# Performance work log

Measured on AMD Instinct MI355X. Metric: run time of the kernel, lower is better.

## Reference

```python
import jax, jax.numpy as jnp
import numpy as np

# B images, N objects/image, R relations/image; D=obj/rel feature dim, H=GGNN hidden,
# NO=num object classes, NR=num relation classes, T=GGNN time steps.
B, N, R, D, H, NO, NR, T = 8, 64, 2048, 4096, 512, 151, 51, 3


def setup_inputs() -> dict:
    key = jax.random.key(0)
    ks = jax.random.split(key, 24)
    nrm = lambda k, shp: jax.random.normal(k, shp, dtype=jnp.float32) * 0.02
    im_inds = jnp.repeat(jnp.arange(B, dtype=jnp.int32), N)          # sorted per-object image ids
    img_r = jnp.repeat(jnp.arange(B, dtype=jnp.int32), R)            # per-relation image ids
    pair = jax.random.randint(ks[0], (B * R, 2), 0, N, dtype=jnp.int32) + (img_r * N)[:, None]
    rel_inds = jnp.concatenate([img_r[:, None], pair], axis=1)        # [B*R, 3]
    return dict(
        im_inds=im_inds, rel_inds=rel_inds,
        obj_fmaps=jax.random.normal(ks[1], (B * N, D), jnp.float32),
        obj_logits=jax.random.normal(ks[2], (B * N, NO), jnp.float32),
        vr=jax.random.normal(ks[3], (B * R, D), jnp.float32),
        W_obj=nrm(ks[4], (D, H)), b_obj=jnp.zeros((H,), jnp.float32),
        W_rel=nrm(ks[5], (D, H)), b_rel=jnp.zeros((H,), jnp.float32),
        W_prob=nrm(ks[6], (NO, H)), b_prob=jnp.zeros((H,), jnp.float32),
        W_so=nrm(ks[7], (H, H)), W_oo=nrm(ks[8], (H, H)),
        W_rs=nrm(ks[9], (H, H)), W_ro=nrm(ks[10], (H, H)),
        Wz=nrm(ks[11], (H, H)), Uz=nrm(ks[12], (H, H)), bz=jnp.zeros((H,), jnp.float32),
        Wr=nrm(ks[13], (H, H)), Ur=nrm(ks[14], (H, H)), br=jnp.zeros((H,), jnp.float32),
        Wh=nrm(ks[15], (H, H)), Uh=nrm(ks[16], (H, H)), bh=jnp.zeros((H,), jnp.float32),
        W_out_rel=nrm(ks[17], (2 * H, H)), b_out_rel=jnp.zeros((H,), jnp.float32),
        W_cls_rel=nrm(ks[18], (H, NR)), b_cls_rel=jnp.zeros((NR,), jnp.float32),
        W_out_obj=nrm(ks[19], (2 * H, H)), b_out_obj=jnp.zeros((H,), jnp.float32),
        W_cls_obj=nrm(ks[20], (H, NO)), b_cls_obj=jnp.zeros((NO,), jnp.float32),
    )


def reference(im_inds, rel_inds, obj_fmaps, obj_logits, vr,
              W_obj, b_obj, W_rel, b_rel, W_prob, b_prob,
              W_so, W_oo, W_rs, W_ro,
              Wz, Uz, bz, Wr, Ur, br, Wh, Uh, bh,
              W_out_rel, b_out_rel, W_cls_rel, b_cls_rel,
              W_out_obj, b_out_obj, W_cls_obj, b_cls_obj):
    # obj_probs = softmax(obj_logits); project features + class distribution into GGNN hidden
    obj_probs = jax.nn.softmax(obj_logits, axis=-1)
    xo = (obj_fmaps @ W_obj + b_obj + obj_probs @ W_prob + b_prob).reshape(B, N, H)
    xr = (vr @ W_rel + b_rel).reshape(B, R, H)
    # per-image local indices: rel_inds[rel_s:rel_e, 1:] - obj_s
    off = (jnp.arange(B, dtype=rel_inds.dtype) * N)[:, None]
    subj = rel_inds[:, 1].reshape(B, R) - off
    objn = rel_inds[:, 2].reshape(B, R) - off

    def gru(h, m):
        z = jax.nn.sigmoid(m @ Wz + h @ Uz + bz)
        r = jax.nn.sigmoid(m @ Wr + h @ Ur + br)
        hh = jnp.tanh(m @ Wh + (r * h) @ Uh + bh)
        return (1.0 - z) * h + z * hh

    def per_image(xo_i, xr_i, s, o):
        ho, hr = xo_i, xr_i
        for _ in range(T):  # fixed recurrence depth (time_step_num)
            mr = ho[s] @ W_so + ho[o] @ W_oo                               # gather obj -> rel
            mo = (jax.ops.segment_sum(hr @ W_rs, s, num_segments=N)
                  + jax.ops.segment_sum(hr @ W_ro, o, num_segments=N))     # scatter rel -> obj
            ho, hr = gru(ho, mo), gru(hr, mr)
        rel_logits = jnp.tanh(jnp.concatenate([hr, xr_i], -1) @ W_out_rel + b_out_rel) @ W_cls_rel + b_cls_rel
        obj_ref = jnp.tanh(jnp.concatenate([ho, xo_i], -1) @ W_out_obj + b_out_obj) @ W_cls_obj + b_cls_obj
        return rel_logits, obj_ref

    rel_logits, obj_ref = jax.vmap(per_image)(xo, xr, subj, objn)
    rel_logits = rel_logits.reshape(B * R, NR)
    obj_ref = obj_ref.reshape(B * N, NO)
    scpred_softmax = jax.nn.softmax(rel_logits, axis=-1)
    scent_softmax = jax.nn.softmax(obj_ref, axis=-1)
    # sgcls, inference, no obj_labels: obj_preds = argmax over classes 1..NO-1, + 1
    obj_preds = jnp.argmax(obj_ref[:, 1:], axis=-1) + 1
    return (obj_ref, obj_preds, rel_logits, scpred_softmax, scent_softmax)
```

## Files before the change

### kernel.cpp

```cpp
#include <hip/hip_runtime.h>
#include <math.h>

#define Bn   8
#define Nn   64
#define Rn   2048
#define Dn   4096
#define Hn   512
#define NOc  151
#define NRc  51
#define Tt   3
#define BNt  (Bn*Nn)
#define BRt  (Bn*Rn)

typedef __attribute__((ext_vector_type(8))) short short8;
typedef __attribute__((ext_vector_type(4))) float f32x4;

__device__ __forceinline__ float sigmf(float x){ return 1.0f/(1.0f+expf(-x)); }

__device__ __forceinline__ ushort f2bf_rne(float x){
  unsigned u = __float_as_uint(x);
  unsigned r = u + 0x7FFFu + ((u>>16)&1u);
  return (ushort)(r>>16);
}

template<int BM,int BN>
__global__ __launch_bounds__(256)
void gemm_b3(const float* __restrict__ A, const ushort* __restrict__ Bhg,
             const ushort* __restrict__ Blg, float* __restrict__ C,
             int M,int N,int K,int lda,int ldb,int ldc,
             const float* __restrict__ bias,int beta,int act)
{
  constexpr int MT = BM/32, NT = BN/32;
  __shared__ ushort Ah[BM*40], Al[BM*40], Bh[BN*40], Bl[BN*40];
  const int tid  = threadIdx.x;
  const int lane = tid & 63;
  const int wid  = tid >> 6;
  const int quad = lane >> 4, l15 = lane & 15;
  const int wm = (wid>>1)*(BM/2), wn = (wid&1)*(BN/2);
  const int bm = blockIdx.y*BM, bn = blockIdx.x*BN;

  constexpr int TPR  = 256/BM;
  constexpr int FPT  = 32/TPR;
  const int ar = tid / TPR;
  const int ak = (tid % TPR) * FPT;
  constexpr int TPRB = 256/BN;
  constexpr int SPT  = 32/TPRB;
  const int br = tid / TPRB;
  const int bk = (tid % TPRB) * SPT;
  const int grA = bm + ar;
  const int grB = bn + br;

  f32x4 acc[MT][NT];
#pragma unroll
  for (int i=0;i<MT;i++)
#pragma unroll
    for (int j=0;j<NT;j++) acc[i][j] = (f32x4){0.f,0.f,0.f,0.f};

  for (int k0=0; k0<K; k0+=32) {
    {
      float av[FPT];
      if (grA < M && k0 + ak + FPT <= K) {
        const float* p = A + (size_t)grA*lda + k0 + ak;
#pragma unroll
        for (int i=0;i<FPT/4;i++) ((float4*)av)[i] = ((const float4*)p)[i];
      } else {
#pragma unroll
        for (int i=0;i<FPT;i++){
          int gk = k0+ak+i;
          av[i] = (grA<M && gk<K) ? A[(size_t)grA*lda+gk] : 0.f;
        }
      }
      ushort hs[FPT], ls[FPT];
#pragma unroll
      for (int i=0;i<FPT;i++){
        ushort h = f2bf_rne(av[i]);
        float hf = __uint_as_float(((unsigned)h)<<16);
        hs[i]=h; ls[i]=f2bf_rne(av[i]-hf);
      }
#pragma unroll
      for (int i=0;i<FPT;i+=8){
        short8 vh, vl;
#pragma unroll
        for (int q=0;q<8;q++){ vh[q]=(short)hs[i+q]; vl[q]=(short)ls[i+q]; }
        *(short8*)&Ah[ar*40+ak+i] = vh;
        *(short8*)&Al[ar*40+ak+i] = vl;
      }
    }
    {
#pragma unroll
      for (int i=0;i<SPT;i+=8){
        short8 vh, vl;
        if (grB < N){
          vh = *(const short8*)(Bhg + (size_t)grB*ldb + k0 + bk + i);
          vl = *(const short8*)(Blg + (size_t)grB*ldb + k0 + bk + i);
        } else {
#pragma unroll
          for (int q=0;q<8;q++){ vh[q]=0; vl[q]=0; }
        }
        *(short8*)&Bh[br*40+bk+i] = vh;
        *(short8*)&Bl[br*40+bk+i] = vl;
      }
    }
    __syncthreads();
    {
      short8 afh[MT], afl[MT], bfh[NT], bfl[NT];
#pragma unroll
      for (int i=0;i<MT;i++){
        int o = (wm + i*16 + l15)*40 + quad*8;
        afh[i] = *(const short8*)&Ah[o];
        afl[i] = *(const short8*)&Al[o];
      }
#pragma unroll
      for (int j=0;j<NT;j++){
        int o = (wn + j*16 + l15)*40 + quad*8;
        bfh[j] = *(const short8*)&Bh[o];
        bfl[j] = *(const short8*)&Bl[o];
      }
#pragma unroll
      for (int i=0;i<MT;i++)
#pragma unroll
        for (int j=0;j<NT;j++)
          acc[i][j] = __builtin_amdgcn_mfma_f32_16x16x32_bf16(afh[i], bfh[j], acc[i][j], 0,0,0);
#pragma unroll
      for (int i=0;i<MT;i++)
#pragma unroll
        for (int j=0;j<NT;j++)
          acc[i][j] = __builtin_amdgcn_mfma_f32_16x16x32_bf16(afh[i], bfl[j], acc[i][j], 0,0,0);
#pragma unroll
      for (int i=0;i<MT;i++)
#pragma unroll
        for (int j=0;j<NT;j++)
          acc[i][j] = __builtin_amdgcn_mfma_f32_16x16x32_bf16(afl[i], bfh[j], acc[i][j], 0,0,0);
    }
    __syncthreads();
  }
#pragma unroll
  for (int i=0;i<MT;i++){
    int gm0 = bm + wm + i*16 + quad*4;
#pragma unroll
    for (int j=0;j<NT;j++){
      int gn = bn + wn + j*16 + l15;
      if (gn >= N) continue;
#pragma unroll
      for (int r=0;r<4;r++){
        int gm = gm0 + r;
        if (gm >= M) continue;
        float v = acc[i][j][r];
        if (beta) v += C[(size_t)gm*ldc+gn];
        if (bias) v += bias[gn];
        if (act==1) v = sigmf(v);
        else if (act==2) v = tanhf(v);
        C[(size_t)gm*ldc+gn] = v;
      }
    }
  }
}

__global__ __launch_bounds__(256)
void tsplit(const float* __restrict__ src,int K,int N,
            ushort* __restrict__ dh, ushort* __restrict__ dl,
            int dld,int rowoff,int koff)
{
  __shared__ float t[32][33];
  const int tx = threadIdx.x, ty = threadIdx.y;
  const int kb = blockIdx.x*32, nb = blockIdx.y*32;
#pragma unroll
  for (int r=0;r<4;r++){
    int k = kb + ty + r*8, n = nb + tx;
    t[ty+r*8][tx] = (k<K && n<N) ? src[(size_t)k*N + n] : 0.f;
  }
  __syncthreads();
#pragma unroll
  for (int r=0;r<4;r++){
    int n = nb + ty + r*8, k = kb + tx;
    if (n < N){
      float v = t[tx][ty+r*8];
      ushort h = f2bf_rne(v);
      float hf = __uint_as_float(((unsigned)h)<<16);
      ushort l = f2bf_rne(v - hf);
      size_t o = (size_t)(rowoff+n)*dld + koff + k;
      dh[o]=h; dl[o]=l;
    }
  }
}

__global__ __launch_bounds__(64)
void softmax_kernel(const float* __restrict__ in, float* __restrict__ out,
                    int cols, int ldi, int ldo, int padto)
{
  int row = blockIdx.x, lane = threadIdx.x;
  const float* rp = in + (size_t)row*ldi;
  float m = -INFINITY;
  for (int c = lane; c < cols; c += 64) m = fmaxf(m, rp[c]);
  for (int off = 32; off; off >>= 1) m = fmaxf(m, __shfl_xor(m, off));
  float s = 0.f;
  for (int c = lane; c < cols; c += 64) s += expf(rp[c]-m);
  for (int off = 32; off; off >>= 1) s += __shfl_xor(s, off);
  float inv = 1.f/s;
  float* op = out + (size_t)row*ldo;
  for (int c = lane; c < padto; c += 64)
    op[c] = (c < cols) ? expf(rp[c]-m)*inv : 0.f;
}

__global__ __launch_bounds__(64)
void argmax_kernel(const float* __restrict__ ref, float* __restrict__ preds)
{
  int row = blockIdx.x, lane = threadIdx.x;
  const float* rp = ref + (size_t)row*NOc;
  float bv = -INFINITY; int bi = NOc;
  for (int c = 1+lane; c < NOc; c += 64) { float v = rp[c]; if (v > bv) { bv=v; bi=c; } }
  for (int off=32; off; off>>=1) {
    float ov = __shfl_xor(bv, off); int oi = __shfl_xor(bi, off);
    if (ov > bv || (ov == bv && oi < bi)) { bv = ov; bi = oi; }
  }
  if (lane==0) preds[row] = (float)bi;
}

__global__ __launch_bounds__(256)
void copy512(float* __restrict__ dst, const float* __restrict__ src, int M)
{
  int i = blockIdx.x*256+threadIdx.x;
  if (i >= M*128) return;
  int row=i>>7, hq=(i&127)<<2;
  *(float4*)&dst[(size_t)row*1024+hq] = *(const float4*)&src[(size_t)row*1024+hq];
}

__global__ __launch_bounds__(64)
void segsum2(const float* __restrict__ HX, const int* __restrict__ rel_inds,
             float* __restrict__ SumSO)
{
  __shared__ float accS[64][64];
  __shared__ float accO[64][64];
  const int t = threadIdx.x;
  const int hb = blockIdx.x*64;
  const int img = blockIdx.z;
  const int relbase = img*Rn + blockIdx.y*(Rn/4);
  for (int ob=0; ob<64; ob++){ accS[ob][t]=0.f; accO[ob][t]=0.f; }
  for (int i=0;i<Rn/4;i++){
    int r = relbase+i;
    int s = rel_inds[r*3+1] - img*64;
    int o = rel_inds[r*3+2] - img*64;
    float v = HX[(size_t)r*1024 + hb + t];
    accS[s][t]+=v; accO[o][t]+=v;
  }
  for (int ob=0;ob<64;ob++){
    size_t rowb = (size_t)(img*64+ob)*1024 + hb + t;
    atomicAdd(&SumSO[rowb],     accS[ob][t]);
    atomicAdd(&SumSO[rowb+512], accO[ob][t]);
  }
}

__global__ __launch_bounds__(256)
void gru_rel_A2(const int* __restrict__ rel, const float* __restrict__ Gso,
                const float* __restrict__ hU, const float* __restrict__ HX,
                const float* __restrict__ bz, const float* __restrict__ br,
                float* __restrict__ Z, float* __restrict__ RH)
{
  int i = blockIdx.x*256 + threadIdx.x;
  if (i >= BRt*128) return;
  int r = i>>7, hq = (i&127)<<2;
  int s = rel[r*3+1], o = rel[r*3+2];
  float4 gzs = *(const float4*)&Gso[(size_t)s*3072 + hq];
  float4 gzo = *(const float4*)&Gso[(size_t)o*3072 + 1536 + hq];
  float4 grs = *(const float4*)&Gso[(size_t)s*3072 + 512 + hq];
  float4 gro = *(const float4*)&Gso[(size_t)o*3072 + 2048 + hq];
  float4 uz  = *(const float4*)&hU[(size_t)r*1024 + hq];
  float4 ur  = *(const float4*)&hU[(size_t)r*1024 + 512 + hq];
  float4 bzv = *(const float4*)&bz[hq];
  float4 brv = *(const float4*)&br[hq];
  float4 hv  = *(const float4*)&HX[(size_t)r*1024 + hq];
  float4 z, rh;
  z.x = sigmf(gzs.x+gzo.x+uz.x+bzv.x);
  z.y = sigmf(gzs.y+gzo.y+uz.y+bzv.y);
  z.z = sigmf(gzs.z+gzo.z+uz.z+bzv.z);
  z.w = sigmf(gzs.w+gzo.w+uz.w+bzv.w);
  rh.x = sigmf(grs.x+gro.x+ur.x+brv.x)*hv.x;
  rh.y = sigmf(grs.y+gro.y+ur.y+brv.y)*hv.y;
  rh.z = sigmf(grs.z+gro.z+ur.z+brv.z)*hv.z;
  rh.w = sigmf(grs.w+gro.w+ur.w+brv.w)*hv.w;
  *(float4*)&Z[(size_t)r*512+hq]  = z;
  *(float4*)&RH[(size_t)r*512+hq] = rh;
}

__global__ __launch_bounds__(256)
void gru_rel_B2(const int* __restrict__ rel, const float* __restrict__ Gso,
                const float* __restrict__ rhU, const float* __restrict__ Z,
                const float* __restrict__ bh, float* __restrict__ HX)
{
  int i = blockIdx.x*256 + threadIdx.x;
  if (i >= BRt*128) return;
  int r = i>>7, hq = (i&127)<<2;
  int s = rel[r*3+1], o = rel[r*3+2];
  float4 ghs = *(const float4*)&Gso[(size_t)s*3072 + 1024 + hq];
  float4 gho = *(const float4*)&Gso[(size_t)o*3072 + 2560 + hq];
  float4 ru  = *(const float4*)&rhU[(size_t)r*512 + hq];
  float4 bhv = *(const float4*)&bh[hq];
  float4 z   = *(const float4*)&Z[(size_t)r*512 + hq];
  float4 hv  = *(const float4*)&HX[(size_t)r*1024 + hq];
  float4 o4;
  o4.x = (1.f-z.x)*hv.x + z.x*tanhf(ghs.x+gho.x+ru.x+bhv.x);
  o4.y = (1.f-z.y)*hv.y + z.y*tanhf(ghs.y+gho.y+ru.y+bhv.y);
  o4.z = (1.f-z.z)*hv.z + z.z*tanhf(ghs.z+gho.z+ru.z+bhv.z);
  o4.w = (1.f-z.w)*hv.w + z.w*tanhf(ghs.w+gho.w+ru.w+bhv.w);
  *(float4*)&HX[(size_t)r*1024+hq] = o4;
}

__global__ __launch_bounds__(256)
void obj_gate(const float* __restrict__ G1, const float* __restrict__ G2,
              const float* __restrict__ HOX, const float* __restrict__ bz,
              const float* __restrict__ br, float* __restrict__ Zo,
              float* __restrict__ RHo)
{
  int i = blockIdx.x*256 + threadIdx.x;
  if (i >= BNt*128) return;
  int row = i>>7, hq = (i&127)<<2;
  float4 g1z = *(const float4*)&G1[(size_t)row*1536 + hq];
  float4 g2z = *(const float4*)&G2[(size_t)row*1024 + hq];
  float4 g1r = *(const float4*)&G1[(size_t)row*1536 + 512 + hq];
  float4 g2r = *(const float4*)&G2[(size_t)row*1024 + 512 + hq];
  float4 bzv = *(const float4*)&bz[hq];
  float4 brv = *(const float4*)&br[hq];
  float4 hv  = *(const float4*)&HOX[(size_t)row*1024 + hq];
  float4 z, rh;
  z.x = sigmf(g1z.x+g2z.x+bzv.x); z.y = sigmf(g1z.y+g2z.y+bzv.y);
  z.z = sigmf(g1z.z+g2z.z+bzv.z); z.w = sigmf(g1z.w+g2z.w+bzv.w);
  rh.x = sigmf(g1r.x+g2r.x+brv.x)*hv.x;
  rh.y = sigmf(g1r.y+g2r.y+brv.y)*hv.y;
  rh.z = sigmf(g1r.z+g2r.z+brv.z)*hv.z;
  rh.w = sigmf(g1r.w+g2r.w+brv.w)*hv.w;
  *(float4*)&Zo[(size_t)row*512+hq]  = z;
  *(float4*)&RHo[(size_t)row*512+hq] = rh;
}

__global__ __launch_bounds__(256)
void obj_upd(const float* __restrict__ G1, const float* __restrict__ rhUo,
             const float* __restrict__ Zo, const float* __restrict__ bh,
             float* __restrict__ HOX)
{
  int i = blockIdx.x*256 + threadIdx.x;
  if (i >= BNt*128) return;
  int row = i>>7, hq = (i&127)<<2;
  float4 g1h = *(const float4*)&G1[(size_t)row*1536 + 1024 + hq];
  float4 ru  = *(const float4*)&rhUo[(size_t)row*512 + hq];
  float4 z   = *(const float4*)&Zo[(size_t)row*512 + hq];
  float4 bhv = *(const float4*)&bh[hq];
  float4 hv  = *(const float4*)&HOX[(size_t)row*1024 + hq];
  float4 o4;
  o4.x = (1.f-z.x)*hv.x + z.x*tanhf(g1h.x+ru.x+bhv.x);
  o4.y = (1.f-z.y)*hv.y + z.y*tanhf(g1h.y+ru.y+bhv.y);
  o4.z = (1.f-z.z)*hv.z + z.z*tanhf(g1h.z+ru.z+bhv.z);
  o4.w = (1.f-z.w)*hv.w + z.w*tanhf(g1h.w+ru.w+bhv.w);
  *(float4*)&HOX[(size_t)row*1024+hq] = o4;
}

static void G128(hipStream_t s,const float*A,const ushort*bh,const ushort*bl,float*C,
  int M,int N,int K,int lda,int ldb,int ldc,const float*bias,int beta,int act){
  dim3 g((N+127)/128,(M+127)/128);
  gemm_b3<128,128><<<g,256,0,s>>>(A,bh,bl,C,M,N,K,lda,ldb,ldc,bias,beta,act);
}
static void G64(hipStream_t s,const float*A,const ushort*bh,const ushort*bl,float*C,
  int M,int N,int K,int lda,int ldb,int ldc,const float*bias,int beta,int act){
  dim3 g((N+63)/64,(M+63)/64);
  gemm_b3<64,64><<<g,256,0,s>>>(A,bh,bl,C,M,N,K,lda,ldb,ldc,bias,beta,act);
}
static void G128x64(hipStream_t s,const float*A,const ushort*bh,const ushort*bl,float*C,
  int M,int N,int K,int lda,int ldb,int ldc,const float*bias,int beta,int act){
  dim3 g((N+63)/64,(M+127)/128);
  gemm_b3<128,64><<<g,256,0,s>>>(A,bh,bl,C,M,N,K,lda,ldb,ldc,bias,beta,act);
}
static void TS(hipStream_t s,const float*src,int K,int N,ushort*dh,ushort*dl,
               int dld,int rowoff,int koff,int Kpad){
  dim3 g(Kpad/32,(N+31)/32);
  tsplit<<<g,dim3(32,8),0,s>>>(src,K,N,dh,dl,dld,rowoff,koff);
}

extern "C" void kernel_launch(void* const* d_in, const int* in_sizes, int n_in,
                              void* d_out, int out_size, void* d_ws, size_t ws_size,
                              hipStream_t stream) {
  (void)in_sizes; (void)n_in; (void)out_size; (void)ws_size;
  const int*   rel_inds   = (const int*)  d_in[1];
  const float* obj_fmaps  = (const float*)d_in[2];
  const float* obj_logits = (const float*)d_in[3];
  const float* vr         = (const float*)d_in[4];
  const float* W_obj      = (const float*)d_in[5];
  const float* b_obj      = (const float*)d_in[6];
  const float* W_rel      = (const float*)d_in[7];
  const float* b_rel      = (const float*)d_in[8];
  const float* W_prob     = (const float*)d_in[9];
  const float* b_prob     = (const float*)d_in[10];
  const float* W_so       = (const float*)d_in[11];
  const float* W_oo       = (const float*)d_in[12];
  const float* W_rs       = (const float*)d_in[13];
  const float* W_ro       = (const float*)d_in[14];
  const float* Wz         = (const float*)d_in[15];
  const float* Uz         = (const float*)d_in[16];
  const float* bz         = (const float*)d_in[17];
  const float* Wr         = (const float*)d_in[18];
  const float* Ur         = (const float*)d_in[19];
  const float* br         = (const float*)d_in[20];
  const float* Wh         = (const float*)d_in[21];
  const float* Uh         = (const float*)d_in[22];
  const float* bh         = (const float*)d_in[23];
  const float* W_out_rel  = (const float*)d_in[24];
  const float* b_out_rel  = (const float*)d_in[25];
  const float* W_cls_rel  = (const float*)d_in[26];
  const float* b_cls_rel  = (const float*)d_in[27];
  const float* W_out_obj  = (const float*)d_in[28];
  const float* b_out_obj  = (const float*)d_in[29];
  const float* W_cls_obj  = (const float*)d_in[30];
  const float* b_cls_obj  = (const float*)d_in[31];

  float* out          = (float*)d_out;
  float* out_obj_ref  = out;
  float* out_preds    = out + 77312;
  float* out_rel_log  = out + 77824;
  float* out_scpred   = out + 913408;
  float* out_scent    = out + 1748992;

  char* base = (char*)d_ws; size_t off = 0;
  auto alloc = [&](size_t bytes)->void*{ void* p = base+off; off = (off+bytes+255)&~(size_t)255; return p; };
  float*  HX    = (float*) alloc((size_t)BRt*1024*4);
  float*  hU    = (float*) alloc((size_t)BRt*1024*4);
  float*  Zb    = (float*) alloc((size_t)BRt*512*4);
  float*  RH    = (float*) alloc((size_t)BRt*512*4);
  ushort* Bt3h  = (ushort*)alloc((size_t)1536*512*2);
  ushort* Bt3l  = (ushort*)alloc((size_t)1536*512*2);
  ushort* BtUh2 = (ushort*)alloc((size_t)1024*512*2);
  ushort* BtUl2 = (ushort*)alloc((size_t)1024*512*2);
  ushort* BtUhh = (ushort*)alloc((size_t)512*512*2);
  ushort* BtUhl = (ushort*)alloc((size_t)512*512*2);
  ushort* BtRRh = (ushort*)alloc((size_t)512*1024*2);
  ushort* BtRRl = (ushort*)alloc((size_t)512*1024*2);
  ushort* BtORh = (ushort*)alloc((size_t)512*1024*2);
  ushort* BtORl = (ushort*)alloc((size_t)512*1024*2);
  ushort* BtCRh = (ushort*)alloc((size_t)51*512*2);
  ushort* BtCRl = (ushort*)alloc((size_t)51*512*2);
  ushort* BtOOh = (ushort*)alloc((size_t)512*1024*2);
  ushort* BtOOl = (ushort*)alloc((size_t)512*1024*2);
  ushort* BtCOh = (ushort*)alloc((size_t)151*512*2);
  ushort* BtCOl = (ushort*)alloc((size_t)151*512*2);
  ushort* BtWCh = (ushort*)alloc((size_t)3072*512*2);
  ushort* BtWCl = (ushort*)alloc((size_t)3072*512*2);
  float*  Gso   = (float*) alloc((size_t)512*3072*4);
  float*  G1    = (float*) alloc((size_t)512*1536*4);
  float*  G2    = (float*) alloc((size_t)512*1024*4);
  float*  SumSO = (float*) alloc((size_t)512*1024*4);
  float*  mo    = (float*) alloc((size_t)512*512*4);
  float*  Zo    = (float*) alloc((size_t)512*512*4);
  float*  RHo   = (float*) alloc((size_t)512*512*4);
  float*  rhUo  = (float*) alloc((size_t)512*512*4);
  float*  HOX   = (float*) alloc((size_t)512*1024*4);
  float*  oprob = (float*) alloc((size_t)512*152*4);
  float*  Cobj  = (float*) alloc((size_t)512*512*4);

  ushort* BtRELh = (ushort*)Zb;
  ushort* BtRELl = BtRELh + (size_t)512*4096;
  ushort* BtOBJh = BtRELl + (size_t)512*4096;
  ushort* BtOBJl = BtOBJh + (size_t)512*4096;
  ushort* BtPRh  = BtOBJl + (size_t)512*4096;
  ushort* BtPRl  = BtPRh  + (size_t)512*160;
  float*  Wcat   = RH;

  softmax_kernel<<<512,64,0,stream>>>(obj_logits, oprob, NOc, NOc, 152, 152);
  TS(stream, W_rel,  4096,512, BtRELh,BtRELl, 4096, 0,0, 4096);
  TS(stream, W_obj,  4096,512, BtOBJh,BtOBJl, 4096, 0,0, 4096);
  TS(stream, W_prob,  151,512, BtPRh, BtPRl,   160, 0,0,  160);
  TS(stream, Wz, 512,512, Bt3h,Bt3l, 512,    0,0, 512);
  TS(stream, Wr, 512,512, Bt3h,Bt3l, 512,  512,0, 512);
  TS(stream, Wh, 512,512, Bt3h,Bt3l, 512, 1024,0, 512);
  TS(stream, Uz, 512,512, BtUh2,BtUl2, 512,   0,0, 512);
  TS(stream, Ur, 512,512, BtUh2,BtUl2, 512, 512,0, 512);
  TS(stream, Uh, 512,512, BtUhh,BtUhl, 512, 0,0, 512);
  TS(stream, W_rs, 512,512, BtRRh,BtRRl, 1024, 0,  0, 512);
  TS(stream, W_ro, 512,512, BtRRh,BtRRl, 1024, 0,512, 512);
  TS(stream, W_out_rel, 1024,512, BtORh,BtORl, 1024, 0,0, 1024);
  TS(stream, W_cls_rel,  512, 51, BtCRh,BtCRl,  512, 0,0,  512);
  TS(stream, W_out_obj, 1024,512, BtOOh,BtOOl, 1024, 0,0, 1024);
  TS(stream, W_cls_obj,  512,151, BtCOh,BtCOl,  512, 0,0,  512);
  G64(stream, obj_fmaps, BtOBJh,BtOBJl, HOX+512, 512,512,4096, 4096,4096,1024, b_obj,0,0);
  G64(stream, oprob,     BtPRh, BtPRl,  HOX+512, 512,512, 151,  152, 160,1024, b_prob,1,0);
  G128(stream, vr, BtRELh,BtRELl, HX+512, BRt,512,4096, 4096,4096,1024, b_rel,0,0);
  copy512<<<(BRt*128+255)/256,256,0,stream>>>(HX, HX+512, BRt);
  copy512<<<(512*128+255)/256,256,0,stream>>>(HOX, HOX+512, 512);
  G64(stream, W_so, Bt3h,Bt3l, Wcat,      512,1536,512, 512,512,3072, nullptr,0,0);
  G64(stream, W_oo, Bt3h,Bt3l, Wcat+1536, 512,1536,512, 512,512,3072, nullptr,0,0);
  TS(stream, Wcat, 512,3072, BtWCh,BtWCl, 512, 0,0, 512);

  for (int t = 0; t < Tt; t++) {
    G64(stream, HOX, BtWCh,BtWCl, Gso, 512,3072,512, 1024,512,3072, nullptr,0,0);
    hipMemsetAsync(SumSO, 0, (size_t)512*1024*4, stream);
    segsum2<<<dim3(8,4,8),64,0,stream>>>(HX, rel_inds, SumSO);
    G128(stream, HX, BtUh2,BtUl2, hU, BRt,1024,512, 1024,512,1024, nullptr,0,0);
    gru_rel_A2<<<(BRt*128+255)/256,256,0,stream>>>(rel_inds, Gso, hU, HX, bz, br, Zb, RH);
    G128(stream, RH, BtUhh,BtUhl, hU , BRt,512,512, 512,512,512, nullptr,0,0);
    gru_rel_B2<<<(BRt*128+255)/256,256,0,stream>>>(rel_inds, Gso, hU, Zb, bh, HX);
    G64(stream, SumSO, BtRRh,BtRRl, mo, 512,512,1024, 1024,1024,512, nullptr,0,0);
    G64(stream, mo,  Bt3h,Bt3l,   G1, 512,1536,512,  512,512,1536, nullptr,0,0);
    G64(stream, HOX, BtUh2,BtUl2, G2, 512,1024,512, 1024,512,1024, nullptr,0,0);
    obj_gate<<<(512*128+255)/256,256,0,stream>>>(G1,G2,HOX,bz,br,Zo,RHo);
    G64(stream, RHo, BtUhh,BtUhl, rhUo, 512,512,512, 512,512,512, nullptr,0,0);
    obj_upd<<<(512*128+255)/256,256,0,stream>>>(G1, rhUo, Zo, bh, HOX);
  }

  float* Crel = hU;
  G128(stream, HX, BtORh,BtORl, Crel, BRt,512,1024, 1024,1024,512, b_out_rel,0,2);
  G128x64(stream, Crel, BtCRh,BtCRl, out_rel_log, BRt,NRc,512, 512,512,NRc, b_cls_rel,0,0);
  softmax_kernel<<<BRt,64,0,stream>>>(out_rel_log, out_scpred, NRc, NRc, NRc, NRc);
  G64(stream, HOX, BtOOh,BtOOl, Cobj, 512,512,1024, 1024,1024,512, b_out_obj,0,2);
  G64(stream, Cobj, BtCOh,BtCOl, out_obj_ref, 512,NOc,512, 512,512,NOc, b_cls_obj,0,0);
  softmax_kernel<<<512,64,0,stream>>>(out_obj_ref, out_scent, NOc, NOc, NOc, NOc);
  argmax_kernel<<<512,64,0,stream>>>(out_obj_ref, out_preds);
}
```

Before: 2.295 ms.

## Fuse GRU gates into GEMM epilogues and merge object/relation rows

```diff
diff --git a/kernel.cpp b/kernel.cpp
--- a/kernel.cpp
+++ b/kernel.cpp
@@ -11,6 +11,7 @@
 #define Tt   3
 #define BNt  (Bn*Nn)
 #define BRt  (Bn*Rn)
+#define Mall (BRt+BNt)
 
 typedef __attribute__((ext_vector_type(8))) short short8;
 typedef __attribute__((ext_vector_type(4))) float f32x4;
@@ -28,7 +29,12 @@
 void gemm_b3(const float* __restrict__ A, const ushort* __restrict__ Bhg,
              const ushort* __restrict__ Blg, float* __restrict__ C,
              int M,int N,int K,int lda,int ldb,int ldc,
-             const float* __restrict__ bias,int beta,int act)
+             const float* __restrict__ bias, const float* __restrict__ bias2,
+             int beta,int act,int dupoff,
+             int mode, const int* __restrict__ rel,
+             const float* __restrict__ Gso, const float* __restrict__ G1,
+             int brt, float* __restrict__ Zbuf, float* __restrict__ RHbuf,
+             float* __restrict__ HXbuf)
 {
   constexpr int MT = BM/32, NT = BN/32;
   __shared__ ushort Ah[BM*40], Al[BM*40], Bh[BN*40], Bl[BN*40];
@@ -45,31 +51,52 @@
   const int ak = (tid % TPR) * FPT;
   constexpr int TPRB = 256/BN;
   constexpr int SPT  = 32/TPRB;
-  const int br = tid / TPRB;
+  const int br_ = tid / TPRB;
   const int bk = (tid % TPRB) * SPT;
   const int grA = bm + ar;
-  const int grB = bn + br;
+  const int grB = bn + br_;
+  const bool avec = ((lda&3)==0);
 
   f32x4 acc[MT][NT];
 #pragma unroll
   for (int i=0;i<MT;i++)
 #pragma unroll
     for (int j=0;j<NT;j++) acc[i][j] = (f32x4){0.f,0.f,0.f,0.f};
+
+  float av[FPT];
+  short8 bvh[SPT/8], bvl[SPT/8];
+
+  auto load_tile = [&](int k0){
+    if (grA < M && avec && k0 + ak + FPT <= K) {
+      const float* p = A + (size_t)grA*lda + k0 + ak;
+#pragma unroll
+      for (int i=0;i<FPT/4;i++) ((float4*)av)[i] = ((const float4*)p)[i];
+    } else {
+#pragma unroll
+      for (int i=0;i<FPT;i++){
+        int gk = k0+ak+i;
+        av[i] = (grA<M && gk<K) ? A[(size_t)grA*lda+gk] : 0.f;
+      }
+    }
+    if (grB < N){
+#pragma unroll
+      for (int i=0;i<SPT/8;i++){
+        bvh[i] = *(const short8*)(Bhg + (size_t)grB*ldb + k0 + bk + i*8);
+        bvl[i] = *(const short8*)(Blg + (size_t)grB*ldb + k0 + bk + i*8);
+      }
+    } else {
+#pragma unroll
+      for (int i=0;i<SPT/8;i++){
+#pragma unroll
+        for (int q=0;q<8;q++){ bvh[i][q]=0; bvl[i][q]=0; }
+      }
+    }
+  };
+
+  load_tile(0);
 
   for (int k0=0; k0<K; k0+=32) {
     {
-      float av[FPT];
-      if (grA < M && k0 + ak + FPT <= K) {
-        const float* p = A + (size_t)grA*lda + k0 + ak;
-#pragma unroll
-        for (int i=0;i<FPT/4;i++) ((float4*)av)[i] = ((const float4*)p)[i];
-      } else {
-#pragma unroll
-        for (int i=0;i<FPT;i++){
-          int gk = k0+ak+i;
-          av[i] = (grA<M && gk<K) ? A[(size_t)grA*lda+gk] : 0.f;
-        }
-      }
       ushort hs[FPT], ls[FPT];
 #pragma unroll
       for (int i=0;i<FPT;i++){
@@ -85,23 +112,14 @@
         *(short8*)&Ah[ar*40+ak+i] = vh;
         *(short8*)&Al[ar*40+ak+i] = vl;
       }
-    }
-    {
-#pragma unroll
-      for (int i=0;i<SPT;i+=8){
-        short8 vh, vl;
-        if (grB < N){
-          vh = *(const short8*)(Bhg + (size_t)grB*ldb + k0 + bk + i);
-          vl = *(const short8*)(Blg + (size_t)grB*ldb + k0 + bk + i);
-        } else {
-#pragma unroll
-          for (int q=0;q<8;q++){ vh[q]=0; vl[q]=0; }
-        }
-        *(short8*)&Bh[br*40+bk+i] = vh;
-        *(short8*)&Bl[br*40+bk+i] = vl;
+#pragma unroll
+      for (int i=0;i<SPT/8;i++){
+        *(short8*)&Bh[br_*40+bk+i*8] = bvh[i];
+        *(short8*)&Bl[br_*40+bk+i*8] = bvl[i];
       }
     }
     __syncthreads();
+    if (k0+32 < K) load_tile(k0+32);
     {
       short8 afh[MT], afl[MT], bfh[NT], bfl[NT];
 #pragma unroll
@@ -134,23 +152,79 @@
     }
     __syncthreads();
   }
-#pragma unroll
-  for (int i=0;i<MT;i++){
-    int gm0 = bm + wm + i*16 + quad*4;
-#pragma unroll
-    for (int j=0;j<NT;j++){
-      int gn = bn + wn + j*16 + l15;
-      if (gn >= N) continue;
+
+  if (mode == 0) {
+#pragma unroll
+    for (int i=0;i<MT;i++){
+      int gm0 = bm + wm + i*16 + quad*4;
+#pragma unroll
+      for (int j=0;j<NT;j++){
+        int gn = bn + wn + j*16 + l15;
+        if (gn >= N) continue;
+#pragma unroll
+        for (int r=0;r<4;r++){
+          int gm = gm0 + r;
+          if (gm >= M) continue;
+          float v = acc[i][j][r];
+          if (beta) v += C[(size_t)gm*ldc+gn];
+          if (bias) v += bias[gn];
+          if (act==1) v = sigmf(v);
+          else if (act==2) v = tanhf(v);
+          C[(size_t)gm*ldc+gn] = v;
+          if (dupoff) C[(size_t)gm*ldc+gn+dupoff] = v;
+        }
+      }
+    }
+  } else if (mode == 1) {
+#pragma unroll
+    for (int i=0;i<MT;i++){
 #pragma unroll
       for (int r=0;r<4;r++){
-        int gm = gm0 + r;
+        int gm = bm + wm + i*16 + quad*4 + r;
         if (gm >= M) continue;
-        float v = acc[i][j][r];
-        if (beta) v += C[(size_t)gm*ldc+gn];
-        if (bias) v += bias[gn];
-        if (act==1) v = sigmf(v);
-        else if (act==2) v = tanhf(v);
-        C[(size_t)gm*ldc+gn] = v;
+        bool isrel = gm < brt;
+        int s=0,o=0; const float* g1row = nullptr;
+        if (isrel){ s = rel[gm*3+1]; o = rel[gm*3+2]; }
+        else g1row = G1 + (size_t)(gm-brt)*1536;
+#pragma unroll
+        for (int j=0;j<NT;j++){
+          int gn = bn + wn + j*16 + l15;
+          float v = acc[i][j][r];
+          if (gn < 512){
+            float g = isrel ? Gso[(size_t)s*3072+gn] + Gso[(size_t)o*3072+1536+gn]
+                            : g1row[gn];
+            Zbuf[(size_t)gm*512+gn] = sigmf(v + g + bias[gn]);
+          } else {
+            int h = gn - 512;
+            float g = isrel ? Gso[(size_t)s*3072+512+h] + Gso[(size_t)o*3072+2048+h]
+                            : g1row[512+h];
+            RHbuf[(size_t)gm*512+h] = sigmf(v + g + bias2[h]) * HXbuf[(size_t)gm*1024+h];
+          }
+        }
+      }
+    }
+  } else {
+#pragma unroll
+    for (int i=0;i<MT;i++){
+#pragma unroll
+      for (int r=0;r<4;r++){
+        int gm = bm + wm + i*16 + quad*4 + r;
+        if (gm >= M) continue;
+        bool isrel = gm < brt;
+        int s=0,o=0; const float* g1row = nullptr;
+        if (isrel){ s = rel[gm*3+1]; o = rel[gm*3+2]; }
+        else g1row = G1 + (size_t)(gm-brt)*1536;
+#pragma unroll
+        for (int j=0;j<NT;j++){
+          int h = bn + wn + j*16 + l15;
+          float v = acc[i][j][r];
+          float g = isrel ? Gso[(size_t)s*3072+1024+h] + Gso[(size_t)o*3072+2560+h]
+                          : g1row[1024+h];
+          float hh = tanhf(v + g + bias[h]);
+          float z = Zbuf[(size_t)gm*512+h];
+          size_t hx = (size_t)gm*1024+h;
+          HXbuf[hx] = (1.f-z)*HXbuf[hx] + z*hh;
+        }
       }
     }
   }
@@ -214,15 +288,6 @@
     if (ov > bv || (ov == bv && oi < bi)) { bv = ov; bi = oi; }
   }
   if (lane==0) preds[row] = (float)bi;
-}
-
-__global__ __launch_bounds__(256)
-void copy512(float* __restrict__ dst, const float* __restrict__ src, int M)
-{
-  int i = blockIdx.x*256+threadIdx.x;
-  if (i >= M*128) return;
-  int row=i>>7, hq=(i&127)<<2;
-  *(float4*)&dst[(size_t)row*1024+hq] = *(const float4*)&src[(size_t)row*1024+hq];
 }
 
 __global__ __launch_bounds__(64)
@@ -250,123 +315,21 @@
   }
 }
 
-__global__ __launch_bounds__(256)
-void gru_rel_A2(const int* __restrict__ rel, const float* __restrict__ Gso,
-                const float* __restrict__ hU, const float* __restrict__ HX,
-                const float* __restrict__ bz, const float* __restrict__ br,
-                float* __restrict__ Z, float* __restrict__ RH)
-{
-  int i = blockIdx.x*256 + threadIdx.x;
-  if (i >= BRt*128) return;
-  int r = i>>7, hq = (i&127)<<2;
-  int s = rel[r*3+1], o = rel[r*3+2];
-  float4 gzs = *(const float4*)&Gso[(size_t)s*3072 + hq];
-  float4 gzo = *(const float4*)&Gso[(size_t)o*3072 + 1536 + hq];
-  float4 grs = *(const float4*)&Gso[(size_t)s*3072 + 512 + hq];
-  float4 gro = *(const float4*)&Gso[(size_t)o*3072 + 2048 + hq];
-  float4 uz  = *(const float4*)&hU[(size_t)r*1024 + hq];
-  float4 ur  = *(const float4*)&hU[(size_t)r*1024 + 512 + hq];
-  float4 bzv = *(const float4*)&bz[hq];
-  float4 brv = *(const float4*)&br[hq];
-  float4 hv  = *(const float4*)&HX[(size_t)r*1024 + hq];
-  float4 z, rh;
-  z.x = sigmf(gzs.x+gzo.x+uz.x+bzv.x);
-  z.y = sigmf(gzs.y+gzo.y+uz.y+bzv.y);
-  z.z = sigmf(gzs.z+gzo.z+uz.z+bzv.z);
-  z.w = sigmf(gzs.w+gzo.w+uz.w+bzv.w);
-  rh.x = sigmf(grs.x+gro.x+ur.x+brv.x)*hv.x;
-  rh.y = sigmf(grs.y+gro.y+ur.y+brv.y)*hv.y;
-  rh.z = sigmf(grs.z+gro.z+ur.z+brv.z)*hv.z;
-  rh.w = sigmf(grs.w+gro.w+ur.w+brv.w)*hv.w;
-  *(float4*)&Z[(size_t)r*512+hq]  = z;
-  *(float4*)&RH[(size_t)r*512+hq] = rh;
-}
-
-__global__ __launch_bounds__(256)
-void gru_rel_B2(const int* __restrict__ rel, const float* __restrict__ Gso,
-                const float* __restrict__ rhU, const float* __restrict__ Z,
-                const float* __restrict__ bh, float* __restrict__ HX)
-{
-  int i = blockIdx.x*256 + threadIdx.x;
-  if (i >= BRt*128) return;
-  int r = i>>7, hq = (i&127)<<2;
-  int s = rel[r*3+1], o = rel[r*3+2];
-  float4 ghs = *(const float4*)&Gso[(size_t)s*3072 + 1024 + hq];
-  float4 gho = *(const float4*)&Gso[(size_t)o*3072 + 2560 + hq];
-  float4 ru  = *(const float4*)&rhU[(size_t)r*512 + hq];
-  float4 bhv = *(const float4*)&bh[hq];
-  float4 z   = *(const float4*)&Z[(size_t)r*512 + hq];
-  float4 hv  = *(const float4*)&HX[(size_t)r*1024 + hq];
-  float4 o4;
-  o4.x = (1.f-z.x)*hv.x + z.x*tanhf(ghs.x+gho.x+ru.x+bhv.x);
-  o4.y = (1.f-z.y)*hv.y + z.y*tanhf(ghs.y+gho.y+ru.y+bhv.y);
-  o4.z = (1.f-z.z)*hv.z + z.z*tanhf(ghs.z+gho.z+ru.z+bhv.z);
-  o4.w = (1.f-z.w)*hv.w + z.w*tanhf(ghs.w+gho.w+ru.w+bhv.w);
-  *(float4*)&HX[(size_t)r*1024+hq] = o4;
-}
-
-__global__ __launch_bounds__(256)
-void obj_gate(const float* __restrict__ G1, const float* __restrict__ G2,
-              const float* __restrict__ HOX, const float* __restrict__ bz,
-              const float* __restrict__ br, float* __restrict__ Zo,
-              float* __restrict__ RHo)
-{
-  int i = blockIdx.x*256 + threadIdx.x;
-  if (i >= BNt*128) return;
-  int row = i>>7, hq = (i&127)<<2;
-  float4 g1z = *(const float4*)&G1[(size_t)row*1536 + hq];
-  float4 g2z = *(const float4*)&G2[(size_t)row*1024 + hq];
-  float4 g1r = *(const float4*)&G1[(size_t)row*1536 + 512 + hq];
-  float4 g2r = *(const float4*)&G2[(size_t)row*1024 + 512 + hq];
-  float4 bzv = *(const float4*)&bz[hq];
-  float4 brv = *(const float4*)&br[hq];
-  float4 hv  = *(const float4*)&HOX[(size_t)row*1024 + hq];
-  float4 z, rh;
-  z.x = sigmf(g1z.x+g2z.x+bzv.x); z.y = sigmf(g1z.y+g2z.y+bzv.y);
-  z.z = sigmf(g1z.z+g2z.z+bzv.z); z.w = sigmf(g1z.w+g2z.w+bzv.w);
-  rh.x = sigmf(g1r.x+g2r.x+brv.x)*hv.x;
-  rh.y = sigmf(g1r.y+g2r.y+brv.y)*hv.y;
-  rh.z = sigmf(g1r.z+g2r.z+brv.z)*hv.z;
-  rh.w = sigmf(g1r.w+g2r.w+brv.w)*hv.w;
-  *(float4*)&Zo[(size_t)row*512+hq]  = z;
-  *(float4*)&RHo[(size_t)row*512+hq] = rh;
-}
-
-__global__ __launch_bounds__(256)
-void obj_upd(const float* __restrict__ G1, const float* __restrict__ rhUo,
-             const float* __restrict__ Zo, const float* __restrict__ bh,
-             float* __restrict__ HOX)
-{
-  int i = blockIdx.x*256 + threadIdx.x;
-  if (i >= BNt*128) return;
-  int row = i>>7, hq = (i&127)<<2;
-  float4 g1h = *(const float4*)&G1[(size_t)row*1536 + 1024 + hq];
-  float4 ru  = *(const float4*)&rhUo[(size_t)row*512 + hq];
-  float4 z   = *(const float4*)&Zo[(size_t)row*512 + hq];
-  float4 bhv = *(const float4*)&bh[hq];
-  float4 hv  = *(const float4*)&HOX[(size_t)row*1024 + hq];
-  float4 o4;
-  o4.x = (1.f-z.x)*hv.x + z.x*tanhf(g1h.x+ru.x+bhv.x);
-  o4.y = (1.f-z.y)*hv.y + z.y*tanhf(g1h.y+ru.y+bhv.y);
-  o4.z = (1.f-z.z)*hv.z + z.z*tanhf(g1h.z+ru.z+bhv.z);
-  o4.w = (1.f-z.w)*hv.w + z.w*tanhf(g1h.w+ru.w+bhv.w);
-  *(float4*)&HOX[(size_t)row*1024+hq] = o4;
-}
-
-static void G128(hipStream_t s,const float*A,const ushort*bh,const ushort*bl,float*C,
-  int M,int N,int K,int lda,int ldb,int ldc,const float*bias,int beta,int act){
+#define NOFUSE 0,nullptr,nullptr,nullptr,0,nullptr,nullptr,nullptr
+static void Gstd128(hipStream_t s,const float*A,const ushort*bh,const ushort*bl,float*C,
+  int M,int N,int K,int lda,int ldb,int ldc,const float*bias,int beta,int act,int dupoff){
   dim3 g((N+127)/128,(M+127)/128);
-  gemm_b3<128,128><<<g,256,0,s>>>(A,bh,bl,C,M,N,K,lda,ldb,ldc,bias,beta,act);
-}
-static void G64(hipStream_t s,const float*A,const ushort*bh,const ushort*bl,float*C,
-  int M,int N,int K,int lda,int ldb,int ldc,const float*bias,int beta,int act){
+  gemm_b3<128,128><<<g,256,0,s>>>(A,bh,bl,C,M,N,K,lda,ldb,ldc,bias,nullptr,beta,act,dupoff,NOFUSE);
+}
+static void Gstd64(hipStream_t s,const float*A,const ushort*bh,const ushort*bl,float*C,
+  int M,int N,int K,int lda,int ldb,int ldc,const float*bias,int beta,int act,int dupoff){
   dim3 g((N+63)/64,(M+63)/64);
-  gemm_b3<64,64><<<g,256,0,s>>>(A,bh,bl,C,M,N,K,lda,ldb,ldc,bias,beta,act);
-}
-static void G128x64(hipStream_t s,const float*A,const ushort*bh,const ushort*bl,float*C,
-  int M,int N,int K,int lda,int ldb,int ldc,const float*bias,int beta,int act){
+  gemm_b3<64,64><<<g,256,0,s>>>(A,bh,bl,C,M,N,K,lda,ldb,ldc,bias,nullptr,beta,act,dupoff,NOFUSE);
+}
+static void Gstd128x64(hipStream_t s,const float*A,const ushort*bh,const ushort*bl,float*C,
+  int M,int N,int K,int lda,int ldb,int ldc,const float*bias,int beta,int act,int dupoff){
   dim3 g((N+63)/64,(M+127)/128);
-  gemm_b3<128,64><<<g,256,0,s>>>(A,bh,bl,C,M,N,K,lda,ldb,ldc,bias,beta,act);
+  gemm_b3<128,64><<<g,256,0,s>>>(A,bh,bl,C,M,N,K,lda,ldb,ldc,bias,nullptr,beta,act,dupoff,NOFUSE);
 }
 static void TS(hipStream_t s,const float*src,int K,int N,ushort*dh,ushort*dl,
                int dld,int rowoff,int koff,int Kpad){
@@ -419,18 +382,17 @@
 
   char* base = (char*)d_ws; size_t off = 0;
   auto alloc = [&](size_t bytes)->void*{ void* p = base+off; off = (off+bytes+255)&~(size_t)255; return p; };
-  float*  HX    = (float*) alloc((size_t)BRt*1024*4);
-  float*  hU    = (float*) alloc((size_t)BRt*1024*4);
-  float*  Zb    = (float*) alloc((size_t)BRt*512*4);
-  float*  RH    = (float*) alloc((size_t)BRt*512*4);
+  float*  HX    = (float*) alloc((size_t)Mall*1024*4);
+  float*  Zb    = (float*) alloc((size_t)Mall*512*4);
+  float*  RH    = (float*) alloc((size_t)Mall*512*4);
   ushort* Bt3h  = (ushort*)alloc((size_t)1536*512*2);
   ushort* Bt3l  = (ushort*)alloc((size_t)1536*512*2);
-  ushort* BtUh2 = (ushort*)alloc((size_t)1024*512*2);
-  ushort* BtUl2 = (ushort*)alloc((size_t)1024*512*2);
-  ushort* BtUhh = (ushort*)alloc((size_t)512*512*2);
-  ushort* BtUhl = (ushort*)alloc((size_t)512*512*2);
-  ushort* BtRRh = (ushort*)alloc((size_t)512*1024*2);
-  ushort* BtRRl = (ushort*)alloc((size_t)512*1024*2);
+  ushort* BtU2h = (ushort*)alloc((size_t)1024*512*2);
+  ushort* BtU2l = (ushort*)alloc((size_t)1024*512*2);
+  ushort* BtUHh = (ushort*)alloc((size_t)512*512*2);
+  ushort* BtUHl = (ushort*)alloc((size_t)512*512*2);
+  ushort* BtPh  = (ushort*)alloc((size_t)1536*1024*2);
+  ushort* BtPl  = (ushort*)alloc((size_t)1536*1024*2);
   ushort* BtORh = (ushort*)alloc((size_t)512*1024*2);
   ushort* BtORl = (ushort*)alloc((size_t)512*1024*2);
   ushort* BtCRh = (ushort*)alloc((size_t)51*512*2);
@@ -443,13 +405,7 @@
   ushort* BtWCl = (ushort*)alloc((size_t)3072*512*2);
   float*  Gso   = (float*) alloc((size_t)512*3072*4);
   float*  G1    = (float*) alloc((size_t)512*1536*4);
-  float*  G2    = (float*) alloc((size_t)512*1024*4);
   float*  SumSO = (float*) alloc((size_t)512*1024*4);
-  float*  mo    = (float*) alloc((size_t)512*512*4);
-  float*  Zo    = (float*) alloc((size_t)512*512*4);
-  float*  RHo   = (float*) alloc((size_t)512*512*4);
-  float*  rhUo  = (float*) alloc((size_t)512*512*4);
-  float*  HOX   = (float*) alloc((size_t)512*1024*4);
   float*  oprob = (float*) alloc((size_t)512*152*4);
   float*  Cobj  = (float*) alloc((size_t)512*512*4);
 
@@ -460,6 +416,9 @@
   ushort* BtPRh  = BtOBJl + (size_t)512*4096;
   ushort* BtPRl  = BtPRh  + (size_t)512*160;
   float*  Wcat   = RH;
+  float*  Pfp    = RH + (size_t)512*3072;
+
+  float* HOXr = HX + (size_t)BRt*1024;
 
   softmax_kernel<<<512,64,0,stream>>>(obj_logits, oprob, NOc, NOc, 152, 152);
   TS(stream, W_rel,  4096,512, BtRELh,BtRELl, 4096, 0,0, 4096);
@@ -468,46 +427,48 @@
   TS(stream, Wz, 512,512, Bt3h,Bt3l, 512,    0,0, 512);
   TS(stream, Wr, 512,512, Bt3h,Bt3l, 512,  512,0, 512);
   TS(stream, Wh, 512,512, Bt3h,Bt3l, 512, 1024,0, 512);
-  TS(stream, Uz, 512,512, BtUh2,BtUl2, 512,   0,0, 512);
-  TS(stream, Ur, 512,512, BtUh2,BtUl2, 512, 512,0, 512);
-  TS(stream, Uh, 512,512, BtUhh,BtUhl, 512, 0,0, 512);
-  TS(stream, W_rs, 512,512, BtRRh,BtRRl, 1024, 0,  0, 512);
-  TS(stream, W_ro, 512,512, BtRRh,BtRRl, 1024, 0,512, 512);
+  TS(stream, Uz, 512,512, BtU2h,BtU2l, 512,   0,0, 512);
+  TS(stream, Ur, 512,512, BtU2h,BtU2l, 512, 512,0, 512);
+  TS(stream, Uh, 512,512, BtUHh,BtUHl, 512, 0,0, 512);
   TS(stream, W_out_rel, 1024,512, BtORh,BtORl, 1024, 0,0, 1024);
   TS(stream, W_cls_rel,  512, 51, BtCRh,BtCRl,  512, 0,0,  512);
   TS(stream, W_out_obj, 1024,512, BtOOh,BtOOl, 1024, 0,0, 1024);
   TS(stream, W_cls_obj,  512,151, BtCOh,BtCOl,  512, 0,0,  512);
-  G64(stream, obj_fmaps, BtOBJh,BtOBJl, HOX+512, 512,512,4096, 4096,4096,1024, b_obj,0,0);
-  G64(stream, oprob,     BtPRh, BtPRl,  HOX+512, 512,512, 151,  152, 160,1024, b_prob,1,0);
-  G128(stream, vr, BtRELh,BtRELl, HX+512, BRt,512,4096, 4096,4096,1024, b_rel,0,0);
-  copy512<<<(BRt*128+255)/256,256,0,stream>>>(HX, HX+512, BRt);
-  copy512<<<(512*128+255)/256,256,0,stream>>>(HOX, HOX+512, 512);
-  G64(stream, W_so, Bt3h,Bt3l, Wcat,      512,1536,512, 512,512,3072, nullptr,0,0);
-  G64(stream, W_oo, Bt3h,Bt3l, Wcat+1536, 512,1536,512, 512,512,3072, nullptr,0,0);
-  TS(stream, Wcat, 512,3072, BtWCh,BtWCl, 512, 0,0, 512);
+  Gstd64(stream, obj_fmaps, BtOBJh,BtOBJl, HOXr+512, 512,512,4096, 4096,4096,1024, b_obj,0,0,0);
+  Gstd64(stream, oprob,     BtPRh, BtPRl,  HOXr+512, 512,512, 151,  152, 160,1024, b_prob,1,0,-512);
+  Gstd128(stream, vr, BtRELh,BtRELl, HX+512, BRt,512,4096, 4096,4096,1024, b_rel,0,0,-512);
+  Gstd64(stream, W_so, Bt3h,Bt3l, Wcat,            512,1536,512, 512,512,3072, nullptr,0,0,0);
+  Gstd64(stream, W_oo, Bt3h,Bt3l, Wcat+1536,       512,1536,512, 512,512,3072, nullptr,0,0,0);
+  Gstd64(stream, W_rs, Bt3h,Bt3l, Pfp,             512,1536,512, 512,512,1536, nullptr,0,0,0);
+  Gstd64(stream, W_ro, Bt3h,Bt3l, Pfp+512*1536,    512,1536,512, 512,512,1536, nullptr,0,0,0);
+  TS(stream, Wcat,  512,3072, BtWCh,BtWCl,  512, 0,0,  512);
+  TS(stream, Pfp,  1024,1536, BtPh, BtPl,  1024, 0,0, 1024);
 
   for (int t = 0; t < Tt; t++) {
-    G64(stream, HOX, BtWCh,BtWCl, Gso, 512,3072,512, 1024,512,3072, nullptr,0,0);
+    Gstd64(stream, HOXr, BtWCh,BtWCl, Gso, 512,3072,512, 1024,512,3072, nullptr,0,0,0);
     hipMemsetAsync(SumSO, 0, (size_t)512*1024*4, stream);
     segsum2<<<dim3(8,4,8),64,0,stream>>>(HX, rel_inds, SumSO);
-    G128(stream, HX, BtUh2,BtUl2, hU, BRt,1024,512, 1024,512,1024, nullptr,0,0);
-    gru_rel_A2<<<(BRt*128+255)/256,256,0,stream>>>(rel_inds, Gso, hU, HX, bz, br, Zb, RH);
-    G128(stream, RH, BtUhh,BtUhl, hU , BRt,512,512, 512,512,512, nullptr,0,0);
-    gru_rel_B2<<<(BRt*128+255)/256,256,0,stream>>>(rel_inds, Gso, hU, Zb, bh, HX);
-    G64(stream, SumSO, BtRRh,BtRRl, mo, 512,512,1024, 1024,1024,512, nullptr,0,0);
-    G64(stream, mo,  Bt3h,Bt3l,   G1, 512,1536,512,  512,512,1536, nullptr,0,0);
-    G64(stream, HOX, BtUh2,BtUl2, G2, 512,1024,512, 1024,512,1024, nullptr,0,0);
-    obj_gate<<<(512*128+255)/256,256,0,stream>>>(G1,G2,HOX,bz,br,Zo,RHo);
-    G64(stream, RHo, BtUhh,BtUhl, rhUo, 512,512,512, 512,512,512, nullptr,0,0);
-    obj_upd<<<(512*128+255)/256,256,0,stream>>>(G1, rhUo, Zo, bh, HOX);
-  }
-
-  float* Crel = hU;
-  G128(stream, HX, BtORh,BtORl, Crel, BRt,512,1024, 1024,1024,512, b_out_rel,0,2);
-  G128x64(stream, Crel, BtCRh,BtCRl, out_rel_log, BRt,NRc,512, 512,512,NRc, b_cls_rel,0,0);
+    Gstd64(stream, SumSO, BtPh,BtPl, G1, 512,1536,1024, 1024,1024,1536, nullptr,0,0,0);
+    {
+      dim3 g(1024/128, Mall/128);
+      gemm_b3<128,128><<<g,256,0,stream>>>(HX, BtU2h,BtU2l, nullptr,
+        Mall,1024,512, 1024,512,0, bz,br,0,0,0,
+        1, rel_inds, Gso, G1, BRt, Zb, RH, HX);
+    }
+    {
+      dim3 g(512/128, Mall/128);
+      gemm_b3<128,128><<<g,256,0,stream>>>(RH, BtUHh,BtUHl, nullptr,
+        Mall,512,512, 512,512,0, bh,nullptr,0,0,0,
+        2, rel_inds, Gso, G1, BRt, Zb, nullptr, HX);
+    }
+  }
+
+  float* Crel = Zb;
+  Gstd128(stream, HX, BtORh,BtORl, Crel, BRt,512,1024, 1024,1024,512, b_out_rel,0,2,0);
+  Gstd128x64(stream, Crel, BtCRh,BtCRl, out_rel_log, BRt,NRc,512, 512,512,NRc, b_cls_rel,0,0,0);
   softmax_kernel<<<BRt,64,0,stream>>>(out_rel_log, out_scpred, NRc, NRc, NRc, NRc);
-  G64(stream, HOX, BtOOh,BtOOl, Cobj, 512,512,1024, 1024,1024,512, b_out_obj,0,2);
-  G64(stream, Cobj, BtCOh,BtCOl, out_obj_ref, 512,NOc,512, 512,512,NOc, b_cls_obj,0,0);
+  Gstd64(stream, HOXr, BtOOh,BtOOl, Cobj, 512,512,1024, 1024,1024,512, b_out_obj,0,2,0);
+  Gstd64(stream, Cobj, BtCOh,BtCOl, out_obj_ref, 512,NOc,512, 512,512,NOc, b_cls_obj,0,0,0);
   softmax_kernel<<<512,64,0,stream>>>(out_obj_ref, out_scent, NOc, NOc, NOc, NOc);
   argmax_kernel<<<512,64,0,stream>>>(out_obj_ref, out_preds);
 }
```

Measured after the change: 2.288 ms. About the same (-0.3%).
